# Kernel tuning notes

Hardware: AMD Instinct MI355X
Metric: run time of the kernel (lower is better)

## Reference

```python
import jax, jax.numpy as jnp
import numpy as np
from jax import lax

NUM_HEADS = 4
DIM_K = 16
DIM_V = 64
EPS = 1e-5  # BatchNorm eps (eval mode, running stats)


def setup_inputs() -> dict:
    key = jax.random.key(0)
    ks = jax.random.split(key, 8)
    B, C, H, W = 32, 256, 32, 32
    out_ch = NUM_HEADS * DIM_K + DIM_K + DIM_V  # 144
    return {
        "x": jax.random.normal(ks[0], (B, C, H, W), jnp.float32),
        "qkv_w": jax.random.normal(ks[1], (out_ch, C), jnp.float32) * (C ** -0.5),
        "q_gamma": jnp.ones((NUM_HEADS * DIM_K,), jnp.float32),
        "q_beta": jnp.zeros((NUM_HEADS * DIM_K,), jnp.float32),
        "q_mean": jax.random.normal(ks[2], (NUM_HEADS * DIM_K,), jnp.float32) * 0.1,
        "q_var": jax.random.uniform(ks[3], (NUM_HEADS * DIM_K,), jnp.float32) + 0.5,
        "v_gamma": jnp.ones((DIM_V,), jnp.float32),
        "v_beta": jnp.zeros((DIM_V,), jnp.float32),
        "v_mean": jax.random.normal(ks[4], (DIM_V,), jnp.float32) * 0.1,
        "v_var": jax.random.uniform(ks[5], (DIM_V,), jnp.float32) + 0.5,
        "lam_w": jax.random.normal(ks[6], (DIM_K, 1, 7, 7, 1), jnp.float32) * (DIM_K ** -0.5),
        "lam_b": jnp.zeros((DIM_K,), jnp.float32),
    }


def _bn(x, gamma, beta, mean, var):
    # eval-mode BatchNorm2d over channel axis 1
    inv = gamma * lax.rsqrt(var + EPS)
    return x * inv[None, :, None, None] + (beta - mean * inv)[None, :, None, None]


def reference(x, qkv_w, q_gamma, q_beta, q_mean, q_var,
              v_gamma, v_beta, v_mean, v_var, lam_w, lam_b):
    B, C, H, W = x.shape
    M = H * W
    nh, dk, dv = NUM_HEADS, DIM_K, DIM_V

    # 1x1 conv == channel matmul
    qkv = jnp.einsum('oc,bchw->bohw', qkv_w, x)
    q = qkv[:, : nh * dk]
    k = qkv[:, nh * dk: nh * dk + dk]
    v = qkv[:, nh * dk + dk:]

    q = _bn(q, q_gamma, q_beta, q_mean, q_var)
    v = _bn(v, v_gamma, v_beta, v_mean, v_var)

    q = jnp.swapaxes(q.reshape(B, nh, dk, M), -1, -2)      # (B, nh, M, dk)
    v = jnp.swapaxes(v.reshape(B, dv, M), -1, -2)          # (B, M, dv)
    k = jax.nn.softmax(k.reshape(B, dk, M), axis=-1)       # softmax over positions

    # content lambda
    content_lam = jnp.einsum('bkm,bmv->bkv', k, v)          # (B, dk, dv)
    content_out = jnp.einsum('bnmk,bkv->bnmv', q, content_lam)

    # position lambda: conv3d over (H, W, dv) with kernel (r, r, 1)
    v_img = v.reshape(B, 1, H, W, dv)
    pos = lax.conv_general_dilated(
        v_img, lam_w, window_strides=(1, 1, 1),
        padding=((3, 3), (3, 3), (0, 0)),
        dimension_numbers=('NCHWD', 'OIHWD', 'NCHWD'))     # (B, dk, H, W, dv)
    pos = pos + lam_b[None, :, None, None, None]
    pos_lam = jnp.swapaxes(pos.reshape(B, dk, M, dv), 1, 2)  # (B, M, dk, dv)
    position_out = jnp.einsum('bnmk,bmkv->bnmv', q, pos_lam)

    out = content_out + position_out                        # (B, nh, M, dv)
    # matches torch .transpose(3, 1).reshape(B, C, H, W)
    out = jnp.swapaxes(out, 1, 3).reshape(B, C, H, W)
    return out
```

## Files before the change

kernel.cpp:

```cpp
#include <hip/hip_runtime.h>
#include <hip/hip_bf16.h>

constexpr int B_ = 32, C_ = 256, H_ = 32, W_ = 32, M_ = 1024;
constexpr int NH = 4, DK = 16, DV = 64;
constexpr float EPS = 1e-5f;

using bf16x8 = __bf16 __attribute__((ext_vector_type(8)));
using f32x4  = float __attribute__((ext_vector_type(4)));

struct alignas(8) Bf4 { __bf16 a, b, c, d; };

__global__ __launch_bounds__(256) void k_qkv(
    const float* __restrict__ x, const float* __restrict__ w,
    const float* __restrict__ qg, const float* __restrict__ qb,
    const float* __restrict__ qm, const float* __restrict__ qv,
    const float* __restrict__ vg, const float* __restrict__ vb,
    const float* __restrict__ vm, const float* __restrict__ vv,
    float* __restrict__ q_out, float* __restrict__ k_out,
    float* __restrict__ v_out)
{
    __shared__ __bf16 xT[64 * 72];
    __shared__ __bf16 wsb[144 * 72];
    __shared__ __align__(16) float ostage[64 * 68];
    __shared__ __align__(16) float inv_s[144];
    __shared__ __align__(16) float add_s[144];

    const int b    = blockIdx.x >> 4;
    const int m0   = (blockIdx.x & 15) * 64;
    const int tid  = threadIdx.x;
    const int wv   = tid >> 6;
    const int lane = tid & 63;
    const int col  = lane & 15;
    const int rowg = lane >> 4;

    if (tid < 144) {
        float iv = 1.f, ad = 0.f;
        if (tid < 64)       { iv = qg[tid] * rsqrtf(qv[tid] + EPS); ad = qb[tid] - qm[tid] * iv; }
        else if (tid >= 80) { int d = tid - 80; iv = vg[d] * rsqrtf(vv[d] + EPS); ad = vb[d] - vm[d] * iv; }
        inv_s[tid] = iv; add_s[tid] = ad;
    }

    f32x4 acc[9];
#pragma unroll
    for (int j = 0; j < 9; j++) acc[j] = (f32x4){0.f, 0.f, 0.f, 0.f};

    for (int c0 = 0; c0 < C_; c0 += 64) {
        __syncthreads();
#pragma unroll
        for (int i = 0; i < 4; i++) {
            int flat = tid + 256 * i;
            int m = flat & 63, c4 = flat >> 6;
            const float* xp = &x[((size_t)b * C_ + c0 + c4 * 4) * M_ + m0 + m];
            float f0 = xp[0], f1 = xp[M_], f2 = xp[2 * M_], f3 = xp[3 * M_];
            Bf4 o{(__bf16)f0, (__bf16)f1, (__bf16)f2, (__bf16)f3};
            *reinterpret_cast<Bf4*>(&xT[m * 72 + c4 * 4]) = o;
        }
#pragma unroll
        for (int i = 0; i < 9; i++) {
            int f4 = tid + 256 * i;
            int o = f4 >> 4, cf = (f4 & 15) * 4;
            float4 wv4 = *reinterpret_cast<const float4*>(&w[o * C_ + c0 + cf]);
            Bf4 ob{(__bf16)wv4.x, (__bf16)wv4.y, (__bf16)wv4.z, (__bf16)wv4.w};
            *reinterpret_cast<Bf4*>(&wsb[o * 72 + cf]) = ob;
        }
        __syncthreads();
#pragma unroll
        for (int ks = 0; ks < 2; ks++) {
            const int cl = ks * 32 + rowg * 8;
            bf16x8 bf = *reinterpret_cast<const bf16x8*>(
                &xT[(16 * wv + col) * 72 + cl]);
#pragma unroll
            for (int j = 0; j < 9; j++) {
                bf16x8 af = *reinterpret_cast<const bf16x8*>(
                    &wsb[(16 * j + col) * 72 + cl]);
                acc[j] = __builtin_amdgcn_mfma_f32_16x16x32_bf16(af, bf, acc[j], 0, 0, 0);
            }
        }
    }

    const int mloc = 16 * wv + col;

    __syncthreads();
#pragma unroll
    for (int j = 0; j < 4; j++)
        *reinterpret_cast<f32x4*>(&ostage[mloc * 68 + 16 * j + rowg * 4]) = acc[j];
    __syncthreads();
#pragma unroll
    for (int i = 0; i < 4; i++) {
        int fl = tid + 256 * i;
        int m = fl >> 4, oc4 = (fl & 15) * 4;
        float4 vr = *reinterpret_cast<const float4*>(&ostage[m * 68 + oc4]);
        float4 iv = *reinterpret_cast<const float4*>(&inv_s[oc4]);
        float4 ad = *reinterpret_cast<const float4*>(&add_s[oc4]);
        float4 rs{vr.x * iv.x + ad.x, vr.y * iv.y + ad.y,
                  vr.z * iv.z + ad.z, vr.w * iv.w + ad.w};
        *reinterpret_cast<float4*>(&q_out[((size_t)b * M_ + m0 + m) * 64 + oc4]) = rs;
    }

    __syncthreads();
#pragma unroll
    for (int r = 0; r < 4; r++)
        ostage[(rowg * 4 + r) * 68 + mloc] = acc[4][r];
    __syncthreads();
    {
        int kk = tid >> 4, m4 = (tid & 15) * 4;
        float4 vr = *reinterpret_cast<const float4*>(&ostage[kk * 68 + m4]);
        *reinterpret_cast<float4*>(&k_out[((size_t)b * DK + kk) * M_ + m0 + m4]) = vr;
    }

    __syncthreads();
#pragma unroll
    for (int j = 5; j < 9; j++)
        *reinterpret_cast<f32x4*>(&ostage[mloc * 68 + 16 * (j - 5) + rowg * 4]) = acc[j];
    __syncthreads();
#pragma unroll
    for (int i = 0; i < 4; i++) {
        int fl = tid + 256 * i;
        int m = fl >> 4, oc4 = (fl & 15) * 4;
        float4 vr = *reinterpret_cast<const float4*>(&ostage[m * 68 + oc4]);
        float4 iv = *reinterpret_cast<const float4*>(&inv_s[80 + oc4]);
        float4 ad = *reinterpret_cast<const float4*>(&add_s[80 + oc4]);
        float4 rs{vr.x * iv.x + ad.x, vr.y * iv.y + ad.y,
                  vr.z * iv.z + ad.z, vr.w * iv.w + ad.w};
        *reinterpret_cast<float4*>(&v_out[((size_t)b * M_ + m0 + m) * 64 + oc4]) = rs;
    }
}

__global__ __launch_bounds__(256) void k_softmax(float* __restrict__ kl)
{
    float4* p4 = reinterpret_cast<float4*>(kl + (size_t)blockIdx.x * M_);
    const int tid = threadIdx.x;
    float4 v = p4[tid];
    float mx = fmaxf(fmaxf(v.x, v.y), fmaxf(v.z, v.w));
#pragma unroll
    for (int off = 32; off >= 1; off >>= 1) mx = fmaxf(mx, __shfl_xor(mx, off));
    __shared__ float red[8];
    if ((tid & 63) == 0) red[tid >> 6] = mx;
    __syncthreads();
    mx = fmaxf(fmaxf(red[0], red[1]), fmaxf(red[2], red[3]));
    v.x = __expf(v.x - mx); v.y = __expf(v.y - mx);
    v.z = __expf(v.z - mx); v.w = __expf(v.w - mx);
    float s = v.x + v.y + v.z + v.w;
#pragma unroll
    for (int off = 32; off >= 1; off >>= 1) s += __shfl_xor(s, off);
    if ((tid & 63) == 0) red[4 + (tid >> 6)] = s;
    __syncthreads();
    s = red[4] + red[5] + red[6] + red[7];
    float inv = 1.f / s;
    v.x *= inv; v.y *= inv; v.z *= inv; v.w *= inv;
    p4[tid] = v;
}

__global__ __launch_bounds__(256) void k_clam(
    const float* __restrict__ ksm, const float* __restrict__ vbn,
    float* __restrict__ clam)
{
    const int b   = blockIdx.x >> 4;
    const int m0  = (blockIdx.x & 15) * 64;
    const int tid = threadIdx.x;
    const int vd  = tid & 63;
    const int kq  = tid >> 6;
    float acc[4] = {0.f, 0.f, 0.f, 0.f};
    for (int mi = 0; mi < 64; mi++) {
        const int m = m0 + mi;
        const float vvv = vbn[(b * M_ + m) * DV + vd];
#pragma unroll
        for (int j = 0; j < 4; j++)
            acc[j] = fmaf(ksm[(b * DK + kq + 4 * j) * M_ + m], vvv, acc[j]);
    }
#pragma unroll
    for (int j = 0; j < 4; j++)
        atomicAdd(&clam[(b * DK + kq + 4 * j) * DV + vd], acc[j]);
}

__global__ __launch_bounds__(512) void k_fuse(
    const float* __restrict__ vbn, const float* __restrict__ qbn,
    const float* __restrict__ clam, const float* __restrict__ lw,
    const float* __restrict__ lb, float* __restrict__ out)
{
    __shared__ float qs[32][68];
    __shared__ float lws[16 * 52];
    __shared__ float s_s[32 * 208];
    __shared__ float ostage[64][132];
    __shared__ float cl_s[16 * 64];
    __shared__ float lb_s[16];

    const int b   = blockIdx.x >> 4;
    const int rt  = blockIdx.x & 15;
    const int h0  = rt * 2;
    const int tid = threadIdx.x;

    for (int i = tid; i < 832; i += 512) {
        int k = i / 52, t = i % 52;
        lws[i] = (t < 49) ? lw[k * 49 + t] : 0.f;
    }
    if (tid < 256)
        *reinterpret_cast<float4*>(&cl_s[tid * 4]) =
            *reinterpret_cast<const float4*>(&clam[b * DK * DV + tid * 4]);
    if (tid < 16) lb_s[tid] = lb[tid];

    const int vd  = tid & 63;
    const int pg  = tid >> 6;
    const int px0 = pg * 4;
    const float* vb_b = vbn + (size_t)b * M_ * DV + vd;

    const int qm_ = tid >> 4, qc4 = (tid & 15) * 4;
    float4 qreg = *reinterpret_cast<const float4*>(
        &qbn[((size_t)b * M_ + h0 * W_ + qm_) * 64 + qc4]);

    for (int grp = 0; grp < 2; grp++) {
        const int mrow = (h0 + grp) * W_;
        *reinterpret_cast<float4*>(&qs[qm_][qc4]) = qreg;
        __syncthreads();

        if (tid < 416) {
            const int m  = tid / 13;
            const int t4 = (tid % 13) * 4;
            f32x4 a0 = {0.f,0.f,0.f,0.f}, a1 = a0, a2 = a0, a3 = a0;
#pragma unroll
            for (int k = 0; k < 16; k++) {
                float4 lw4 = *reinterpret_cast<const float4*>(&lws[k * 52 + t4]);
                float q0 = qs[m][k],      q1 = qs[m][16 + k];
                float q2 = qs[m][32 + k], q3 = qs[m][48 + k];
                a0[0] = fmaf(q0, lw4.x, a0[0]); a0[1] = fmaf(q1, lw4.x, a0[1]);
                a0[2] = fmaf(q2, lw4.x, a0[2]); a0[3] = fmaf(q3, lw4.x, a0[3]);
                a1[0] = fmaf(q0, lw4.y, a1[0]); a1[1] = fmaf(q1, lw4.y, a1[1]);
                a1[2] = fmaf(q2, lw4.y, a1[2]); a1[3] = fmaf(q3, lw4.y, a1[3]);
                a2[0] = fmaf(q0, lw4.z, a2[0]); a2[1] = fmaf(q1, lw4.z, a2[1]);
                a2[2] = fmaf(q2, lw4.z, a2[2]); a2[3] = fmaf(q3, lw4.z, a2[3]);
                a3[0] = fmaf(q0, lw4.w, a3[0]); a3[1] = fmaf(q1, lw4.w, a3[1]);
                a3[2] = fmaf(q2, lw4.w, a3[2]); a3[3] = fmaf(q3, lw4.w, a3[3]);
            }
            float* sp = &s_s[m * 208 + t4 * 4];
            *reinterpret_cast<f32x4*>(sp)      = a0;
            *reinterpret_cast<f32x4*>(sp + 4)  = a1;
            *reinterpret_cast<f32x4*>(sp + 8)  = a2;
            *reinterpret_cast<f32x4*>(sp + 12) = a3;
        }
        __syncthreads();

        if (grp == 0)
            qreg = *reinterpret_cast<const float4*>(
                &qbn[((size_t)b * M_ + (h0 + 1) * W_ + qm_) * 64 + qc4]);

        float po[4][4];
#pragma unroll
        for (int ip = 0; ip < 4; ip++)
#pragma unroll
            for (int n = 0; n < 4; n++) po[ip][n] = 0.f;

        float vrC[10], vrN[10];
        {
            const int gr = h0 + grp - 3;
            if (gr >= 0 && gr < H_) {
#pragma unroll
                for (int j = 0; j < 10; j++) {
                    const int colc = px0 - 3 + j;
                    vrC[j] = (colc >= 0 && colc < W_)
                           ? vb_b[(size_t)(gr * W_ + colc) * DV] : 0.f;
                }
            } else {
#pragma unroll
                for (int j = 0; j < 10; j++) vrC[j] = 0.f;
            }
        }
#pragma unroll 1
        for (int dy = 0; dy < 7; dy++) {
            const int grn = h0 + grp - 2 + dy;
            if (dy < 6 && grn >= 0 && grn < H_) {
#pragma unroll
                for (int j = 0; j < 10; j++) {
                    const int colc = px0 - 3 + j;
                    vrN[j] = (colc >= 0 && colc < W_)
                           ? vb_b[(size_t)(grn * W_ + colc) * DV] : 0.f;
                }
            } else {
#pragma unroll
                for (int j = 0; j < 10; j++) vrN[j] = 0.f;
            }
#pragma unroll
            for (int dx = 0; dx < 7; dx++) {
                const int tap = dy * 7 + dx;
#pragma unroll
                for (int ip = 0; ip < 4; ip++) {
                    float4 s4 = *reinterpret_cast<const float4*>(
                        &s_s[(px0 + ip) * 208 + tap * 4]);
                    const float vv = vrC[ip + dx];
                    po[ip][0] = fmaf(vv, s4.x, po[ip][0]);
                    po[ip][1] = fmaf(vv, s4.y, po[ip][1]);
                    po[ip][2] = fmaf(vv, s4.z, po[ip][2]);
                    po[ip][3] = fmaf(vv, s4.w, po[ip][3]);
                }
            }
#pragma unroll
            for (int j = 0; j < 10; j++) vrC[j] = vrN[j];
        }

        float lamv[16];
#pragma unroll
        for (int k = 0; k < 16; k++)
            lamv[k] = cl_s[k * DV + vd] + lb_s[k];
#pragma unroll
        for (int ip = 0; ip < 4; ip++) {
            const int p = px0 + ip;
            float4 ov;
            float* ovp = reinterpret_cast<float*>(&ov);
#pragma unroll
            for (int n = 0; n < 4; n++) {
                const float4* q4 = reinterpret_cast<const float4*>(&qs[p][n * 16]);
                float4 qa = q4[0], qb4 = q4[1], qc = q4[2], qd = q4[3];
                ovp[n] = po[ip][n]
                       + qa.x * lamv[0] + qa.y * lamv[1] + qa.z * lamv[2] + qa.w * lamv[3]
                       + qb4.x * lamv[4] + qb4.y * lamv[5] + qb4.z * lamv[6] + qb4.w * lamv[7]
                       + qc.x * lamv[8] + qc.y * lamv[9] + qc.z * lamv[10] + qc.w * lamv[11]
                       + qd.x * lamv[12] + qd.y * lamv[13] + qd.z * lamv[14] + qd.w * lamv[15];
            }
            *reinterpret_cast<float4*>(&ostage[vd][p * 4]) = ov;
        }
        __syncthreads();
        {
            const int mrow4 = mrow * 4;
            for (int i4 = tid; i4 < 2048; i4 += 512) {
                const int vdw  = i4 >> 5;
                const int off4 = (i4 & 31) * 4;
                float4 val = *reinterpret_cast<const float4*>(&ostage[vdw][off4]);
                *reinterpret_cast<float4*>(
                    out + (size_t)b * (C_ * M_) + (size_t)vdw * 4096 + mrow4 + off4) = val;
            }
        }
        __syncthreads();
    }
}

extern "C" void kernel_launch(void* const* d_in, const int* in_sizes, int n_in,
                              void* d_out, int out_size, void* d_ws, size_t ws_size,
                              hipStream_t stream)
{
    (void)in_sizes; (void)n_in; (void)out_size; (void)ws_size;
    const float* x   = (const float*)d_in[0];
    const float* w   = (const float*)d_in[1];
    const float* qg  = (const float*)d_in[2];
    const float* qb  = (const float*)d_in[3];
    const float* qm  = (const float*)d_in[4];
    const float* qvr = (const float*)d_in[5];
    const float* vg  = (const float*)d_in[6];
    const float* vb  = (const float*)d_in[7];
    const float* vm  = (const float*)d_in[8];
    const float* vvr = (const float*)d_in[9];
    const float* lw  = (const float*)d_in[10];
    const float* lb  = (const float*)d_in[11];
    float* out = (float*)d_out;

    float* ws   = (float*)d_ws;
    float* q_bn = ws;
    float* v_bn = ws + 2097152;
    float* k_bf = ws + 4194304;
    float* clam = ws + 4718592;

    hipMemsetAsync(clam, 0, 32768 * sizeof(float), stream);
    hipLaunchKernelGGL(k_qkv, dim3(512), dim3(256), 0, stream,
                       x, w, qg, qb, qm, qvr, vg, vb, vm, vvr, q_bn, k_bf, v_bn);
    hipLaunchKernelGGL(k_softmax, dim3(512), dim3(256), 0, stream, k_bf);
    hipLaunchKernelGGL(k_clam, dim3(512), dim3(256), 0, stream, k_bf, v_bn, clam);
    hipLaunchKernelGGL(k_fuse, dim3(512), dim3(512), 0, stream,
                       v_bn, q_bn, clam, lw, lb, out);
}
```

Before: 89.65 us.

## Fuse key softmax into content-lambda kernel and drop atomics and memset

Merges the softmax and content-lambda kernels. Each block normalizes one (batch, key) row, keeps the probabilities in shared memory, and computes that row's 64-wide content lambda directly, so the separate memset and atomicAdd accumulation go away. This removes one kernel launch, a memset, the write-back and re-read of the softmaxed keys, and atomic traffic. In exchange, each block now reads the full 1024x64 V slice for its batch, so V is re-read 16 times per batch, once for each key row.

```diff
diff --git a/kernel.cpp b/kernel.cpp
--- a/kernel.cpp
+++ b/kernel.cpp
@@ -126,15 +126,23 @@
     }
 }
 
-__global__ __launch_bounds__(256) void k_softmax(float* __restrict__ kl)
+__global__ __launch_bounds__(256) void k_sc(
+    const float* __restrict__ klog, const float* __restrict__ vbn,
+    float* __restrict__ clam)
 {
-    float4* p4 = reinterpret_cast<float4*>(kl + (size_t)blockIdx.x * M_);
+    __shared__ float p_s[1024];
+    __shared__ float red[8];
+    __shared__ float part[4][64];
+
+    const int bk  = blockIdx.x;
+    const int b   = bk >> 4;
     const int tid = threadIdx.x;
+
+    const float4* p4 = reinterpret_cast<const float4*>(klog + (size_t)bk * M_);
     float4 v = p4[tid];
     float mx = fmaxf(fmaxf(v.x, v.y), fmaxf(v.z, v.w));
 #pragma unroll
     for (int off = 32; off >= 1; off >>= 1) mx = fmaxf(mx, __shfl_xor(mx, off));
-    __shared__ float red[8];
     if ((tid & 63) == 0) red[tid >> 6] = mx;
     __syncthreads();
     mx = fmaxf(fmaxf(red[0], red[1]), fmaxf(red[2], red[3]));
@@ -146,31 +154,24 @@
     if ((tid & 63) == 0) red[4 + (tid >> 6)] = s;
     __syncthreads();
     s = red[4] + red[5] + red[6] + red[7];
-    float inv = 1.f / s;
+    const float inv = 1.f / s;
     v.x *= inv; v.y *= inv; v.z *= inv; v.w *= inv;
-    p4[tid] = v;
-}
-
-__global__ __launch_bounds__(256) void k_clam(
-    const float* __restrict__ ksm, const float* __restrict__ vbn,
-    float* __restrict__ clam)
-{
-    const int b   = blockIdx.x >> 4;
-    const int m0  = (blockIdx.x & 15) * 64;
-    const int tid = threadIdx.x;
-    const int vd  = tid & 63;
-    const int kq  = tid >> 6;
-    float acc[4] = {0.f, 0.f, 0.f, 0.f};
-    for (int mi = 0; mi < 64; mi++) {
-        const int m = m0 + mi;
-        const float vvv = vbn[(b * M_ + m) * DV + vd];
-#pragma unroll
-        for (int j = 0; j < 4; j++)
-            acc[j] = fmaf(ksm[(b * DK + kq + 4 * j) * M_ + m], vvv, acc[j]);
-    }
-#pragma unroll
-    for (int j = 0; j < 4; j++)
-        atomicAdd(&clam[(b * DK + kq + 4 * j) * DV + vd], acc[j]);
+    *reinterpret_cast<float4*>(&p_s[tid * 4]) = v;
+    __syncthreads();
+
+    const int vd = tid & 63;
+    const int qr = tid >> 6;
+    const float* vp = vbn + ((size_t)b * M_ + qr * 256) * DV + vd;
+    const float* pq = &p_s[qr * 256];
+    float acc = 0.f;
+#pragma unroll 8
+    for (int i = 0; i < 256; i++)
+        acc = fmaf(pq[i], vp[(size_t)i * DV], acc);
+    part[qr][vd] = acc;
+    __syncthreads();
+    if (tid < 64)
+        clam[(size_t)bk * DV + tid] =
+            part[0][tid] + part[1][tid] + part[2][tid] + part[3][tid];
 }
 
 __global__ __launch_bounds__(512) void k_fuse(
@@ -357,11 +358,9 @@
     float* k_bf = ws + 4194304;
     float* clam = ws + 4718592;
 
-    hipMemsetAsync(clam, 0, 32768 * sizeof(float), stream);
     hipLaunchKernelGGL(k_qkv, dim3(512), dim3(256), 0, stream,
                        x, w, qg, qb, qm, qvr, vg, vb, vm, vvr, q_bn, k_bf, v_bn);
-    hipLaunchKernelGGL(k_softmax, dim3(512), dim3(256), 0, stream, k_bf);
-    hipLaunchKernelGGL(k_clam, dim3(512), dim3(256), 0, stream, k_bf, v_bn, clam);
+    hipLaunchKernelGGL(k_sc, dim3(512), dim3(256), 0, stream, k_bf, v_bn, clam);
     hipLaunchKernelGGL(k_fuse, dim3(512), dim3(512), 0, stream,
                        v_bn, q_bn, clam, lw, lb, out);
 }
```

Measured after the change: 85.66 us. 1.05x faster.
